# Kernel tuning notes

Measured on AMD Instinct MI355X. Metric: run time of the kernel, lower is better.

## Reference

```python
import jax, jax.numpy as jnp
import numpy as np

# OGB full_atom_feature_dims
FEAT_DIMS = np.array([119, 5, 12, 12, 10, 6, 6, 2, 2], dtype=np.int32)
OFFSETS = jnp.asarray(np.concatenate([[0], np.cumsum(FEAT_DIMS)[:-1]]), dtype=jnp.int32)  # [9]
TOTAL_ROWS = int(FEAT_DIMS.sum())  # 174
DIM = 256
N_CLASS = 10
B, MAX_NODE = 128, 1024


def setup_inputs() -> dict:
    key = jax.random.key(0)
    ks = jax.random.split(key, 16)
    # per-field valid categorical indices, stacked -> [B, MAX_NODE, 9]
    cols = [jax.random.randint(ks[i], (B, MAX_NODE), 0, int(FEAT_DIMS[i]), dtype=jnp.int32)
            for i in range(9)]
    node_feat = jnp.stack(cols, axis=-1)
    num_nodes = jax.random.randint(ks[9], (B,), 1, MAX_NODE + 1, dtype=jnp.int32)
    rxn_class = jax.random.randint(ks[10], (B,), 0, N_CLASS, dtype=jnp.int32)
    # learned params
    atom_emb = jax.random.normal(ks[11], (TOTAL_ROWS, DIM), dtype=jnp.float32) * 0.02
    rxn_emb = jax.random.normal(ks[12], (N_CLASS, DIM), dtype=jnp.float32) * 0.02
    lin_w = jax.random.normal(ks[13], (DIM, 2 * DIM), dtype=jnp.float32) * (1.0 / np.sqrt(2 * DIM))
    lin_b = jax.random.normal(ks[14], (DIM,), dtype=jnp.float32) * 0.01
    return {"node_feat": node_feat, "num_nodes": num_nodes, "rxn_class": rxn_class,
            "atom_emb": atom_emb, "rxn_emb": rxn_emb, "lin_w": lin_w, "lin_b": lin_b}


def reference(node_feat, num_nodes, rxn_class, atom_emb, rxn_emb, lin_w, lin_b):
    # AtomEncoder: sum of 9 per-field embedding lookups (tables concatenated with offsets)
    idx = node_feat + OFFSETS  # [B, N, 9]
    enc = atom_emb[idx].sum(axis=2)  # [B, N, dim]
    # zero-pad positions beyond num_nodes (ragged-to-dense scatter)
    mask = (jnp.arange(MAX_NODE)[None, :] < num_nodes[:, None])[..., None]  # [B, N, 1]
    enc = jnp.where(mask, enc, jnp.zeros((), dtype=enc.dtype))
    # class embedding broadcast over all node slots (including padding, as in original)
    cls = jnp.broadcast_to(rxn_emb[rxn_class][:, None, :], enc.shape)  # [B, N, dim]
    h = jnp.concatenate([enc, cls], axis=-1)  # [B, N, 2*dim]
    out = jnp.einsum('bnd,od->bno', h, lin_w) + lin_b  # [B, N, dim]
    return out
```

## Files before the change

kernel.cpp:

```cpp
#include <hip/hip_runtime.h>
#include <stdint.h>

#define BATCH 128
#define MAXN 1024
#define NF 9
#define DIM 256
#define NCLS 10

#define BASE1 119
#define BASE2 179
#define BASE3 299
#define QROWS 443

typedef __attribute__((ext_vector_type(4))) float f32x4;

__global__ __launch_bounds__(256) void prep_kernel(
    const float* __restrict__ rxn_emb, const float* __restrict__ lin_w,
    const float* __restrict__ lin_b, const float* __restrict__ atom_emb,
    float* __restrict__ Q, float* __restrict__ clsT)
{
  __shared__ float S[4][DIM];
  const int bid = blockIdx.x;
  const int t = threadIdx.x;
  const bool isCls = bid < 3;
  const int row0 = isCls ? bid * 4 : (bid - 3) * 4;
  const int rmax = isCls ? NCLS : QROWS;
  const int nrows = (row0 + 4 <= rmax) ? 4 : (rmax - row0);

#pragma unroll
  for (int r = 0; r < 4; ++r) {
    float v = 0.f;
    if (r < nrows) {
      const int q = row0 + r;
      if (isCls) {
        v = rxn_emb[q * DIM + t];
      } else if (q < BASE1) {
        v = atom_emb[q * DIM + t];
      } else if (q < BASE2) {
        int x = q - BASE1;
        v = atom_emb[(119 + x / 12) * DIM + t] + atom_emb[(124 + x % 12) * DIM + t];
      } else if (q < BASE3) {
        int x = q - BASE2;
        v = atom_emb[(136 + x / 10) * DIM + t] + atom_emb[(148 + x % 10) * DIM + t];
      } else {
        int x = q - BASE3;
        int i8 = x & 1, i7 = (x >> 1) & 1, y = x >> 2;
        v = atom_emb[(158 + y / 6) * DIM + t] + atom_emb[(164 + y % 6) * DIM + t]
          + atom_emb[(170 + i7) * DIM + t] + atom_emb[(172 + i8) * DIM + t];
      }
    }
    S[r][t] = v;
  }
  __syncthreads();

  const float* wrow = lin_w + (size_t)t * 2 * DIM + (isCls ? DIM : 0);
  const float init = isCls ? lin_b[t] : 0.f;
  float a0 = init, a1 = init, a2 = init, a3 = init;
#pragma unroll 4
  for (int d = 0; d < DIM; d += 4) {
    float4 w4 = *(const float4*)(wrow + d);
    a0 += w4.x * S[0][d] + w4.y * S[0][d + 1] + w4.z * S[0][d + 2] + w4.w * S[0][d + 3];
    a1 += w4.x * S[1][d] + w4.y * S[1][d + 1] + w4.z * S[1][d + 2] + w4.w * S[1][d + 3];
    a2 += w4.x * S[2][d] + w4.y * S[2][d + 1] + w4.z * S[2][d + 2] + w4.w * S[2][d + 3];
    a3 += w4.x * S[3][d] + w4.y * S[3][d + 1] + w4.z * S[3][d + 2] + w4.w * S[3][d + 3];
  }
  float* dst = isCls ? clsT : Q;
  if (0 < nrows) dst[(row0 + 0) * DIM + t] = a0;
  if (1 < nrows) dst[(row0 + 1) * DIM + t] = a1;
  if (2 < nrows) dst[(row0 + 2) * DIM + t] = a2;
  if (3 < nrows) dst[(row0 + 3) * DIM + t] = a3;
}

__global__ __launch_bounds__(256, 4) void main_kernel(
    const int* __restrict__ node_feat, const int* __restrict__ num_nodes,
    const int* __restrict__ rxn_class,
    const float* __restrict__ Q, const float* __restrict__ clsT,
    float* __restrict__ out)
{
  const int tid = threadIdx.x;
  const int lane = tid & 63;
  const int w = __builtin_amdgcn_readfirstlane(tid >> 6);
  const int wid = blockIdx.x * 4 + w;
  const int b = wid >> 6;
  const int n0 = (wid & 63) << 4;
  const int nn = num_nodes[b];

  const f32x4 cf = ((const f32x4*)clsT)[rxn_class[b] * 64 + lane];
  f32x4* __restrict__ outp = (f32x4*)out + ((size_t)(b * MAXN + n0)) * 64 + lane;

  if (n0 >= nn) {
#pragma unroll
    for (int i = 0; i < 16; ++i)
      __builtin_nontemporal_store(cf, outp + i * 64);
    return;
  }

  const int* __restrict__ p = node_feat + (size_t)(b * MAXN + n0) * NF;
  const f32x4* __restrict__ Q4 = (const f32x4*)Q;

  if (n0 + 16 <= nn) {
#pragma unroll 4
    for (int i = 0; i < 16; ++i) {
      const int j0 = p[i * NF + 0];
      const int j1 = BASE1 + p[i * NF + 1] * 12 + p[i * NF + 2];
      const int j2 = BASE2 + p[i * NF + 3] * 10 + p[i * NF + 4];
      const int j3 = BASE3 + ((p[i * NF + 5] * 6 + p[i * NF + 6]) * 2 + p[i * NF + 7]) * 2 + p[i * NF + 8];
      const f32x4 v0 = Q4[j0 * 64 + lane];
      const f32x4 v1 = Q4[j1 * 64 + lane];
      const f32x4 v2 = Q4[j2 * 64 + lane];
      const f32x4 v3 = Q4[j3 * 64 + lane];
      const f32x4 s = (v0 + v1) + (v2 + v3);
      __builtin_nontemporal_store(cf + s, outp + i * 64);
    }
    return;
  }

#pragma unroll 4
  for (int i = 0; i < 16; ++i) {
    const int j0 = p[i * NF + 0];
    const int j1 = BASE1 + p[i * NF + 1] * 12 + p[i * NF + 2];
    const int j2 = BASE2 + p[i * NF + 3] * 10 + p[i * NF + 4];
    const int j3 = BASE3 + ((p[i * NF + 5] * 6 + p[i * NF + 6]) * 2 + p[i * NF + 7]) * 2 + p[i * NF + 8];
    const f32x4 v0 = Q4[j0 * 64 + lane];
    const f32x4 v1 = Q4[j1 * 64 + lane];
    const f32x4 v2 = Q4[j2 * 64 + lane];
    const f32x4 v3 = Q4[j3 * 64 + lane];
    const float m = (n0 + i < nn) ? 1.f : 0.f;
    const f32x4 s = (v0 + v1) + (v2 + v3);
    __builtin_nontemporal_store(cf + m * s, outp + i * 64);
  }
}

extern "C" void kernel_launch(void* const* d_in, const int* in_sizes, int n_in,
                              void* d_out, int out_size, void* d_ws, size_t ws_size,
                              hipStream_t stream) {
  const int* node_feat = (const int*)d_in[0];
  const int* num_nodes = (const int*)d_in[1];
  const int* rxn_class = (const int*)d_in[2];
  const float* atom_emb = (const float*)d_in[3];
  const float* rxn_emb = (const float*)d_in[4];
  const float* lin_w = (const float*)d_in[5];
  const float* lin_b = (const float*)d_in[6];
  float* outp = (float*)d_out;

  float* Q = (float*)d_ws;
  float* clsT = (float*)((char*)d_ws + QROWS * DIM * sizeof(float));

  const int nQblocks = (QROWS + 3) / 4;
  prep_kernel<<<3 + nQblocks, 256, 0, stream>>>(rxn_emb, lin_w, lin_b,
                                                atom_emb, Q, clsT);
  main_kernel<<<2048, 256, 0, stream>>>(node_feat, num_nodes, rxn_class,
                                        Q, clsT, outp);
}
```

Measured before the change: 45.92 us.

## Store projected embedding table in bf16 and halve rows per prep block

The precomputed projected-embedding table Q is now rounded to bf16 in the prep kernel, and the main kernel loads it with 8-byte nontemporal loads and widens to fp32 before summing. The prep kernel handles 2 rows per block instead of 4, so it launches more blocks, and the occupancy hint on the main kernel is dropped. The intent is to cut gather bandwidth and cache footprint for the table, at the cost of bf16 rounding error in the output, which may exceed the reference tolerance.

```diff
diff --git a/kernel.cpp b/kernel.cpp
--- a/kernel.cpp
+++ b/kernel.cpp
@@ -13,22 +13,38 @@
 #define QROWS 443
 
 typedef __attribute__((ext_vector_type(4))) float f32x4;
+typedef __attribute__((ext_vector_type(2))) uint32_t u32x2;
+
+__device__ __forceinline__ ushort f32_to_bf16_rne(float x) {
+  uint32_t u = __float_as_uint(x);
+  u += 0x7fffu + ((u >> 16) & 1u);
+  return (ushort)(u >> 16);
+}
+
+__device__ __forceinline__ f32x4 bf4_to_f32x4(u32x2 v) {
+  f32x4 r;
+  r.x = __uint_as_float(v.x << 16);
+  r.y = __uint_as_float(v.x & 0xffff0000u);
+  r.z = __uint_as_float(v.y << 16);
+  r.w = __uint_as_float(v.y & 0xffff0000u);
+  return r;
+}
 
 __global__ __launch_bounds__(256) void prep_kernel(
     const float* __restrict__ rxn_emb, const float* __restrict__ lin_w,
     const float* __restrict__ lin_b, const float* __restrict__ atom_emb,
-    float* __restrict__ Q, float* __restrict__ clsT)
+    ushort* __restrict__ Qb, float* __restrict__ clsT)
 {
-  __shared__ float S[4][DIM];
+  __shared__ float S[2][DIM];
   const int bid = blockIdx.x;
   const int t = threadIdx.x;
-  const bool isCls = bid < 3;
-  const int row0 = isCls ? bid * 4 : (bid - 3) * 4;
+  const bool isCls = bid < 5;
+  const int row0 = isCls ? bid * 2 : (bid - 5) * 2;
   const int rmax = isCls ? NCLS : QROWS;
-  const int nrows = (row0 + 4 <= rmax) ? 4 : (rmax - row0);
+  const int nrows = (rmax - row0 < 2) ? (rmax - row0) : 2;
 
 #pragma unroll
-  for (int r = 0; r < 4; ++r) {
+  for (int r = 0; r < 2; ++r) {
     float v = 0.f;
     if (r < nrows) {
       const int q = row0 + r;
@@ -55,26 +71,26 @@
 
   const float* wrow = lin_w + (size_t)t * 2 * DIM + (isCls ? DIM : 0);
   const float init = isCls ? lin_b[t] : 0.f;
-  float a0 = init, a1 = init, a2 = init, a3 = init;
+  float a0 = init, a1 = init;
 #pragma unroll 4
   for (int d = 0; d < DIM; d += 4) {
     float4 w4 = *(const float4*)(wrow + d);
     a0 += w4.x * S[0][d] + w4.y * S[0][d + 1] + w4.z * S[0][d + 2] + w4.w * S[0][d + 3];
     a1 += w4.x * S[1][d] + w4.y * S[1][d + 1] + w4.z * S[1][d + 2] + w4.w * S[1][d + 3];
-    a2 += w4.x * S[2][d] + w4.y * S[2][d + 1] + w4.z * S[2][d + 2] + w4.w * S[2][d + 3];
-    a3 += w4.x * S[3][d] + w4.y * S[3][d + 1] + w4.z * S[3][d + 2] + w4.w * S[3][d + 3];
   }
-  float* dst = isCls ? clsT : Q;
-  if (0 < nrows) dst[(row0 + 0) * DIM + t] = a0;
-  if (1 < nrows) dst[(row0 + 1) * DIM + t] = a1;
-  if (2 < nrows) dst[(row0 + 2) * DIM + t] = a2;
-  if (3 < nrows) dst[(row0 + 3) * DIM + t] = a3;
+  if (isCls) {
+    clsT[row0 * DIM + t] = a0;
+    if (nrows > 1) clsT[(row0 + 1) * DIM + t] = a1;
+  } else {
+    Qb[row0 * DIM + t] = f32_to_bf16_rne(a0);
+    if (nrows > 1) Qb[(row0 + 1) * DIM + t] = f32_to_bf16_rne(a1);
+  }
 }
 
-__global__ __launch_bounds__(256, 4) void main_kernel(
+__global__ __launch_bounds__(256) void main_kernel(
     const int* __restrict__ node_feat, const int* __restrict__ num_nodes,
     const int* __restrict__ rxn_class,
-    const float* __restrict__ Q, const float* __restrict__ clsT,
+    const ushort* __restrict__ Qb, const float* __restrict__ clsT,
     float* __restrict__ out)
 {
   const int tid = threadIdx.x;
@@ -96,7 +112,7 @@
   }
 
   const int* __restrict__ p = node_feat + (size_t)(b * MAXN + n0) * NF;
-  const f32x4* __restrict__ Q4 = (const f32x4*)Q;
+  const u32x2* __restrict__ Q2 = (const u32x2*)Qb;
 
   if (n0 + 16 <= nn) {
 #pragma unroll 4
@@ -105,11 +121,12 @@
       const int j1 = BASE1 + p[i * NF + 1] * 12 + p[i * NF + 2];
       const int j2 = BASE2 + p[i * NF + 3] * 10 + p[i * NF + 4];
       const int j3 = BASE3 + ((p[i * NF + 5] * 6 + p[i * NF + 6]) * 2 + p[i * NF + 7]) * 2 + p[i * NF + 8];
-      const f32x4 v0 = Q4[j0 * 64 + lane];
-      const f32x4 v1 = Q4[j1 * 64 + lane];
-      const f32x4 v2 = Q4[j2 * 64 + lane];
-      const f32x4 v3 = Q4[j3 * 64 + lane];
-      const f32x4 s = (v0 + v1) + (v2 + v3);
+      const u32x2 v0 = __builtin_nontemporal_load(Q2 + j0 * 64 + lane);
+      const u32x2 v1 = __builtin_nontemporal_load(Q2 + j1 * 64 + lane);
+      const u32x2 v2 = __builtin_nontemporal_load(Q2 + j2 * 64 + lane);
+      const u32x2 v3 = __builtin_nontemporal_load(Q2 + j3 * 64 + lane);
+      const f32x4 s = (bf4_to_f32x4(v0) + bf4_to_f32x4(v1))
+                    + (bf4_to_f32x4(v2) + bf4_to_f32x4(v3));
       __builtin_nontemporal_store(cf + s, outp + i * 64);
     }
     return;
@@ -121,12 +138,13 @@
     const int j1 = BASE1 + p[i * NF + 1] * 12 + p[i * NF + 2];
     const int j2 = BASE2 + p[i * NF + 3] * 10 + p[i * NF + 4];
     const int j3 = BASE3 + ((p[i * NF + 5] * 6 + p[i * NF + 6]) * 2 + p[i * NF + 7]) * 2 + p[i * NF + 8];
-    const f32x4 v0 = Q4[j0 * 64 + lane];
-    const f32x4 v1 = Q4[j1 * 64 + lane];
-    const f32x4 v2 = Q4[j2 * 64 + lane];
-    const f32x4 v3 = Q4[j3 * 64 + lane];
+    const u32x2 v0 = __builtin_nontemporal_load(Q2 + j0 * 64 + lane);
+    const u32x2 v1 = __builtin_nontemporal_load(Q2 + j1 * 64 + lane);
+    const u32x2 v2 = __builtin_nontemporal_load(Q2 + j2 * 64 + lane);
+    const u32x2 v3 = __builtin_nontemporal_load(Q2 + j3 * 64 + lane);
     const float m = (n0 + i < nn) ? 1.f : 0.f;
-    const f32x4 s = (v0 + v1) + (v2 + v3);
+    const f32x4 s = (bf4_to_f32x4(v0) + bf4_to_f32x4(v1))
+                  + (bf4_to_f32x4(v2) + bf4_to_f32x4(v3));
     __builtin_nontemporal_store(cf + m * s, outp + i * 64);
   }
 }
@@ -143,12 +161,11 @@
   const float* lin_b = (const float*)d_in[6];
   float* outp = (float*)d_out;
 
-  float* Q = (float*)d_ws;
-  float* clsT = (float*)((char*)d_ws + QROWS * DIM * sizeof(float));
+  ushort* Qb = (ushort*)d_ws;
+  float* clsT = (float*)((char*)d_ws + QROWS * DIM * sizeof(ushort));
 
-  const int nQblocks = (QROWS + 3) / 4;
-  prep_kernel<<<3 + nQblocks, 256, 0, stream>>>(rxn_emb, lin_w, lin_b,
-                                                atom_emb, Q, clsT);
+  prep_kernel<<<5 + (QROWS + 1) / 2, 256, 0, stream>>>(rxn_emb, lin_w, lin_b,
+                                                       atom_emb, Qb, clsT);
   main_kernel<<<2048, 256, 0, stream>>>(node_feat, num_nodes, rxn_class,
-                                        Q, clsT, outp);
+                                        Qb, clsT, outp);
 }
```

New measurement: 70.69 us. +53.9%, slower.
